# Optimization experiments

Measured on AMD Instinct MI355X. Metric: run time of the kernel, lower is better.

The kernel has to match this reference:

```python
import jax, jax.numpy as jnp
import numpy as np

N_NODES = 50000
N_EDGES = 400000
D_IN = 512
D_OUT = 512


def setup_inputs() -> dict:
    key = jax.random.key(0)
    k1, k2, k3, k4, k5 = jax.random.split(key, 5)
    x = jax.random.normal(k1, (N_NODES, D_IN), dtype=jnp.float32)
    adj_rows = jax.random.randint(k2, (N_EDGES,), 0, N_NODES, dtype=jnp.int32)
    adj_cols = jax.random.randint(k3, (N_EDGES,), 0, N_NODES, dtype=jnp.int32)
    adj_vals = jax.random.uniform(k4, (N_EDGES,), dtype=jnp.float32)
    # Xavier uniform init for weight, zeros for bias (as in reset_parameters)
    limit = float(np.sqrt(6.0 / (D_IN + D_OUT)))
    weight = jax.random.uniform(k5, (D_IN, D_OUT), minval=-limit, maxval=limit, dtype=jnp.float32)
    bias = jnp.zeros((D_OUT,), dtype=jnp.float32)
    return {"x": x, "adj_rows": adj_rows, "adj_cols": adj_cols,
            "adj_vals": adj_vals, "weight": weight, "bias": bias}


def reference(x, adj_rows, adj_cols, adj_vals, weight, bias):
    # support = x @ W  : dense GEMM [N, D_in] x [D_in, D_out]
    support = jnp.matmul(x, weight)
    # output = spmm(adj, support): COO sparse-dense matmul via gather + segment_sum
    messages = adj_vals[:, None] * support[adj_cols]  # [E, D_out]
    output = jax.ops.segment_sum(messages, adj_rows, num_segments=N_NODES)
    return output + bias
```

## Files before the change

### kernel.cpp

```cpp
#include <hip/hip_runtime.h>

#define N_NODES 50000
#define N_EDGES 400000
#define DIM 512
#define NPAD 50048
#define MTILES 391
#define NTILES 4
#define LDP 40

typedef short  short8  __attribute__((ext_vector_type(8)));
typedef unsigned short ushort8 __attribute__((ext_vector_type(8)));
typedef float  f32x4   __attribute__((ext_vector_type(4)));

__device__ __forceinline__ unsigned short f2bf(float f) {
    unsigned int u = __float_as_uint(f);
    u += 0x7fffu + ((u >> 16) & 1u);
    return (unsigned short)(u >> 16);
}
__device__ __forceinline__ float bf2f(unsigned short h) {
    return __uint_as_float(((unsigned int)h) << 16);
}

__global__ __launch_bounds__(256) void cast_x_kernel(const float* __restrict__ x,
                                                     unsigned short* __restrict__ xb) {
    size_t t = (size_t)blockIdx.x * 256 + threadIdx.x;
    size_t base = t * 8;
    int row = (int)(base >> 9);
    ushort8 o;
    if (row < N_NODES) {
        f32x4 a = *(const f32x4*)(x + base);
        f32x4 b = *(const f32x4*)(x + base + 4);
        o[0] = f2bf(a[0]); o[1] = f2bf(a[1]); o[2] = f2bf(a[2]); o[3] = f2bf(a[3]);
        o[4] = f2bf(b[0]); o[5] = f2bf(b[1]); o[6] = f2bf(b[2]); o[7] = f2bf(b[3]);
    } else {
        #pragma unroll
        for (int q = 0; q < 8; ++q) o[q] = 0;
    }
    *(ushort8*)(xb + base) = o;
}

__global__ __launch_bounds__(256) void cast_wt_kernel(const float* __restrict__ w,
                                                      unsigned short* __restrict__ wt) {
    int t = blockIdx.x * 256 + threadIdx.x;
    int n = t >> 9, k = t & 511;
    wt[t] = f2bf(w[k * 512 + n]);
}

__global__ __launch_bounds__(256) void hist_kernel(const int* __restrict__ rows,
                                                   int* __restrict__ counts) {
    int e = blockIdx.x * 256 + threadIdx.x;
    if (e < N_EDGES) atomicAdd(&counts[rows[e]], 1);
}

__global__ __launch_bounds__(512) void scan_blocks_kernel(const int* __restrict__ counts,
                                                          int* __restrict__ tmp,
                                                          int* __restrict__ partials) {
    __shared__ int sm[512];
    int i = blockIdx.x * 512 + threadIdx.x;
    int v = (i < N_NODES) ? counts[i] : 0;
    sm[threadIdx.x] = v;
    __syncthreads();
    #pragma unroll
    for (int off = 1; off < 512; off <<= 1) {
        int val = 0;
        if ((int)threadIdx.x >= off) val = sm[threadIdx.x - off];
        __syncthreads();
        if ((int)threadIdx.x >= off) sm[threadIdx.x] += val;
        __syncthreads();
    }
    if (i < N_NODES) tmp[i] = sm[threadIdx.x] - v;
    if (threadIdx.x == 511) partials[blockIdx.x] = sm[511];
}

__global__ __launch_bounds__(128) void scan_partials_kernel(int* __restrict__ partials) {
    __shared__ int sm[128];
    const int nb = 98;
    int v = ((int)threadIdx.x < nb) ? partials[threadIdx.x] : 0;
    sm[threadIdx.x] = v;
    __syncthreads();
    #pragma unroll
    for (int off = 1; off < 128; off <<= 1) {
        int val = 0;
        if ((int)threadIdx.x >= off) val = sm[threadIdx.x - off];
        __syncthreads();
        if ((int)threadIdx.x >= off) sm[threadIdx.x] += val;
        __syncthreads();
    }
    if ((int)threadIdx.x < nb) partials[threadIdx.x] = sm[threadIdx.x] - v;
}

__global__ __launch_bounds__(256) void add_offsets_kernel(const int* __restrict__ tmp,
                                                          const int* __restrict__ partials,
                                                          int* __restrict__ row_start,
                                                          int* __restrict__ cursor) {
    int i = blockIdx.x * 256 + threadIdx.x;
    if (i < N_NODES) {
        int rs = tmp[i] + partials[i >> 9];
        row_start[i] = rs;
        cursor[i] = rs;
    }
}

__global__ __launch_bounds__(256) void scatter_kernel(const int* __restrict__ rows,
                                                      const int* __restrict__ cols,
                                                      const float* __restrict__ vals,
                                                      int* __restrict__ cursor,
                                                      int* __restrict__ csr_col,
                                                      float* __restrict__ csr_val) {
    int e = blockIdx.x * 256 + threadIdx.x;
    if (e < N_EDGES) {
        int r = rows[e];
        int p = atomicAdd(&cursor[r], 1);
        csr_col[p] = cols[e];
        csr_val[p] = vals[e];
    }
}

__global__ __launch_bounds__(256) void gemm_kernel(const unsigned short* __restrict__ Xb,
                                                   const unsigned short* __restrict__ Wt,
                                                   unsigned short* __restrict__ S) {
    __shared__ __align__(16) unsigned short As[128 * LDP];
    __shared__ __align__(16) unsigned short Bs[128 * LDP];
    const int m0 = blockIdx.y * 128;
    const int n0 = blockIdx.x * 128;
    const int t = threadIdx.x;
    const int lane = t & 63;
    const int w = t >> 6;
    const int wr = w >> 1, wc = w & 1;
    const int fr = lane & 15;
    const int kg = lane >> 4;

    f32x4 acc[4][4];
    #pragma unroll
    for (int i = 0; i < 4; ++i)
        #pragma unroll
        for (int j = 0; j < 4; ++j)
            #pragma unroll
            for (int q = 0; q < 4; ++q) acc[i][j][q] = 0.0f;

    const int c0 = t, c1 = t + 256;
    const int ar0 = c0 >> 2, ak0 = c0 & 3;
    const int ar1 = c1 >> 2, ak1 = c1 & 3;

    for (int kk = 0; kk < DIM; kk += 32) {
        __syncthreads();
        *(f32x4*)&As[ar0 * LDP + ak0 * 8] = *(const f32x4*)&Xb[(size_t)(m0 + ar0) * DIM + kk + ak0 * 8];
        *(f32x4*)&As[ar1 * LDP + ak1 * 8] = *(const f32x4*)&Xb[(size_t)(m0 + ar1) * DIM + kk + ak1 * 8];
        *(f32x4*)&Bs[ar0 * LDP + ak0 * 8] = *(const f32x4*)&Wt[(size_t)(n0 + ar0) * DIM + kk + ak0 * 8];
        *(f32x4*)&Bs[ar1 * LDP + ak1 * 8] = *(const f32x4*)&Wt[(size_t)(n0 + ar1) * DIM + kk + ak1 * 8];
        __syncthreads();

        short8 af[4], bf[4];
        #pragma unroll
        for (int mi = 0; mi < 4; ++mi)
            af[mi] = *(const short8*)&As[(wr * 64 + mi * 16 + fr) * LDP + kg * 8];
        #pragma unroll
        for (int ni = 0; ni < 4; ++ni)
            bf[ni] = *(const short8*)&Bs[(wc * 64 + ni * 16 + fr) * LDP + kg * 8];

        #pragma unroll
        for (int mi = 0; mi < 4; ++mi)
            #pragma unroll
            for (int ni = 0; ni < 4; ++ni)
                acc[mi][ni] = __builtin_amdgcn_mfma_f32_16x16x32_bf16(af[mi], bf[ni], acc[mi][ni], 0, 0, 0);
    }

    #pragma unroll
    for (int mi = 0; mi < 4; ++mi) {
        #pragma unroll
        for (int ni = 0; ni < 4; ++ni) {
            int gr = m0 + wr * 64 + mi * 16 + kg * 4;
            int gc = n0 + wc * 64 + ni * 16 + fr;
            #pragma unroll
            for (int j = 0; j < 4; ++j)
                S[(size_t)(gr + j) * DIM + gc] = f2bf(acc[mi][ni][j]);
        }
    }
}

__global__ __launch_bounds__(64) void spmm_kernel(const unsigned short* __restrict__ S,
                                                  const int* __restrict__ row_start,
                                                  const int* __restrict__ counts,
                                                  const int* __restrict__ csr_col,
                                                  const float* __restrict__ csr_val,
                                                  const float* __restrict__ bias,
                                                  float* __restrict__ out) {
    const int r = blockIdx.x;
    const int lane = threadIdx.x;
    const int s = row_start[r];
    const int n = counts[r];
    float acc[8];
    #pragma unroll
    for (int q = 0; q < 8; ++q) acc[q] = 0.0f;

    for (int j = 0; j < n; ++j) {
        int c = csr_col[s + j];
        float v = csr_val[s + j];
        ushort8 sv = *(const ushort8*)&S[(size_t)c * DIM + lane * 8];
        #pragma unroll
        for (int q = 0; q < 8; ++q) acc[q] += v * bf2f(sv[q]);
    }
    #pragma unroll
    for (int q = 0; q < 8; ++q) acc[q] += bias[lane * 8 + q];

    f32x4 o0, o1;
    #pragma unroll
    for (int q = 0; q < 4; ++q) { o0[q] = acc[q]; o1[q] = acc[4 + q]; }
    *(f32x4*)&out[(size_t)r * DIM + lane * 8] = o0;
    *(f32x4*)&out[(size_t)r * DIM + lane * 8 + 4] = o1;
}

extern "C" void kernel_launch(void* const* d_in, const int* in_sizes, int n_in,
                              void* d_out, int out_size, void* d_ws, size_t ws_size,
                              hipStream_t stream) {
    const float* x    = (const float*)d_in[0];
    const int*   rows = (const int*)d_in[1];
    const int*   cols = (const int*)d_in[2];
    const float* vals = (const float*)d_in[3];
    const float* w    = (const float*)d_in[4];
    const float* bias = (const float*)d_in[5];
    float* out = (float*)d_out;

    char* ws = (char*)d_ws;
    size_t off = 0;
    auto alloc = [&](size_t bytes) -> char* {
        char* p = ws + off;
        off = (off + bytes + 255) & ~(size_t)255;
        return p;
    };
    unsigned short* Xb      = (unsigned short*)alloc((size_t)NPAD * DIM * 2);
    unsigned short* Wt      = (unsigned short*)alloc((size_t)DIM * DIM * 2);
    unsigned short* S       = (unsigned short*)alloc((size_t)NPAD * DIM * 2);
    int*            counts  = (int*)alloc((size_t)N_NODES * 4);
    int*            tmp     = (int*)alloc((size_t)N_NODES * 4);
    int*            rstart  = (int*)alloc((size_t)N_NODES * 4);
    int*            cursor  = (int*)alloc((size_t)N_NODES * 4);
    int*            partials= (int*)alloc(512);
    int*            csr_col = (int*)alloc((size_t)N_EDGES * 4);
    float*          csr_val = (float*)alloc((size_t)N_EDGES * 4);

    hipMemsetAsync(counts, 0, (size_t)N_NODES * 4, stream);

    cast_x_kernel<<<(NPAD * DIM / 8) / 256, 256, 0, stream>>>(x, Xb);
    cast_wt_kernel<<<(DIM * DIM) / 256, 256, 0, stream>>>(w, Wt);

    hist_kernel<<<(N_EDGES + 255) / 256, 256, 0, stream>>>(rows, counts);
    scan_blocks_kernel<<<98, 512, 0, stream>>>(counts, tmp, partials);
    scan_partials_kernel<<<1, 128, 0, stream>>>(partials);
    add_offsets_kernel<<<(N_NODES + 255) / 256, 256, 0, stream>>>(tmp, partials, rstart, cursor);
    scatter_kernel<<<(N_EDGES + 255) / 256, 256, 0, stream>>>(rows, cols, vals, cursor, csr_col, csr_val);

    gemm_kernel<<<dim3(NTILES, MTILES), 256, 0, stream>>>(Xb, Wt, S);
    spmm_kernel<<<N_NODES, 64, 0, stream>>>(S, rstart, counts, csr_col, csr_val, bias, out);
}
```

Baseline: 356.6 us.

## Use direct global-to-LDS loads in GEMM, pack CSR pairs, unroll SpMM gathers

The GEMM now stages tiles with global_load_lds straight into unpadded LDS instead of going through registers, and moves the barrier to the end of each k-step. The CSR column and value arrays are interleaved into one int2 array, and the SpMM loop is unrolled by four so four independent row gathers are in flight at once, with out-of-range slots masked to column 0 and value 0. Output stores become nontemporal. Without padding, LDS reads in the GEMM may hit bank conflicts, and the unrolled loop reads up to three entries past a row's end, which the extra allocation padding is meant to cover.

```diff
diff --git a/kernel.cpp b/kernel.cpp
--- a/kernel.cpp
+++ b/kernel.cpp
@@ -6,11 +6,14 @@
 #define NPAD 50048
 #define MTILES 391
 #define NTILES 4
-#define LDP 40
 
 typedef short  short8  __attribute__((ext_vector_type(8)));
 typedef unsigned short ushort8 __attribute__((ext_vector_type(8)));
 typedef float  f32x4   __attribute__((ext_vector_type(4)));
+typedef int    int2v   __attribute__((ext_vector_type(2)));
+
+typedef __attribute__((address_space(1))) const unsigned short gu16;
+typedef __attribute__((address_space(3))) unsigned short lu16;
 
 __device__ __forceinline__ unsigned short f2bf(float f) {
     unsigned int u = __float_as_uint(f);
@@ -105,22 +108,23 @@
                                                       const int* __restrict__ cols,
                                                       const float* __restrict__ vals,
                                                       int* __restrict__ cursor,
-                                                      int* __restrict__ csr_col,
-                                                      float* __restrict__ csr_val) {
+                                                      int2v* __restrict__ csr_cv) {
     int e = blockIdx.x * 256 + threadIdx.x;
     if (e < N_EDGES) {
         int r = rows[e];
         int p = atomicAdd(&cursor[r], 1);
-        csr_col[p] = cols[e];
-        csr_val[p] = vals[e];
+        int2v cv;
+        cv[0] = cols[e];
+        cv[1] = __float_as_int(vals[e]);
+        csr_cv[p] = cv;
     }
 }
 
 __global__ __launch_bounds__(256) void gemm_kernel(const unsigned short* __restrict__ Xb,
                                                    const unsigned short* __restrict__ Wt,
                                                    unsigned short* __restrict__ S) {
-    __shared__ __align__(16) unsigned short As[128 * LDP];
-    __shared__ __align__(16) unsigned short Bs[128 * LDP];
+    __shared__ __align__(16) unsigned short As[128 * 32];
+    __shared__ __align__(16) unsigned short Bs[128 * 32];
     const int m0 = blockIdx.y * 128;
     const int n0 = blockIdx.x * 128;
     const int t = threadIdx.x;
@@ -138,31 +142,39 @@
             #pragma unroll
             for (int q = 0; q < 4; ++q) acc[i][j][q] = 0.0f;
 
-    const int c0 = t, c1 = t + 256;
-    const int ar0 = c0 >> 2, ak0 = c0 & 3;
-    const int ar1 = c1 >> 2, ak1 = c1 & 3;
+    const int row0 = w * 16 + (lane >> 2);
+    const int row1 = row0 + 64;
+    const int col0 = (lane & 3) * 8;
+    lu16* AsW = (lu16*)(As + w * 512);
+    lu16* BsW = (lu16*)(Bs + w * 512);
+
+    const unsigned short* gA0 = Xb + (size_t)(m0 + row0) * DIM + col0;
+    const unsigned short* gA1 = Xb + (size_t)(m0 + row1) * DIM + col0;
+    const unsigned short* gB0 = Wt + (size_t)(n0 + row0) * DIM + col0;
+    const unsigned short* gB1 = Wt + (size_t)(n0 + row1) * DIM + col0;
 
     for (int kk = 0; kk < DIM; kk += 32) {
-        __syncthreads();
-        *(f32x4*)&As[ar0 * LDP + ak0 * 8] = *(const f32x4*)&Xb[(size_t)(m0 + ar0) * DIM + kk + ak0 * 8];
-        *(f32x4*)&As[ar1 * LDP + ak1 * 8] = *(const f32x4*)&Xb[(size_t)(m0 + ar1) * DIM + kk + ak1 * 8];
-        *(f32x4*)&Bs[ar0 * LDP + ak0 * 8] = *(const f32x4*)&Wt[(size_t)(n0 + ar0) * DIM + kk + ak0 * 8];
-        *(f32x4*)&Bs[ar1 * LDP + ak1 * 8] = *(const f32x4*)&Wt[(size_t)(n0 + ar1) * DIM + kk + ak1 * 8];
+        __builtin_amdgcn_global_load_lds((gu16*)(gA0 + kk), AsW,        16, 0, 0);
+        __builtin_amdgcn_global_load_lds((gu16*)(gA1 + kk), AsW + 2048, 16, 0, 0);
+        __builtin_amdgcn_global_load_lds((gu16*)(gB0 + kk), BsW,        16, 0, 0);
+        __builtin_amdgcn_global_load_lds((gu16*)(gB1 + kk), BsW + 2048, 16, 0, 0);
         __syncthreads();
 
         short8 af[4], bf[4];
         #pragma unroll
         for (int mi = 0; mi < 4; ++mi)
-            af[mi] = *(const short8*)&As[(wr * 64 + mi * 16 + fr) * LDP + kg * 8];
+            af[mi] = *(const short8*)&As[(wr * 64 + mi * 16 + fr) * 32 + kg * 8];
         #pragma unroll
         for (int ni = 0; ni < 4; ++ni)
-            bf[ni] = *(const short8*)&Bs[(wc * 64 + ni * 16 + fr) * LDP + kg * 8];
+            bf[ni] = *(const short8*)&Bs[(wc * 64 + ni * 16 + fr) * 32 + kg * 8];
 
         #pragma unroll
         for (int mi = 0; mi < 4; ++mi)
             #pragma unroll
             for (int ni = 0; ni < 4; ++ni)
                 acc[mi][ni] = __builtin_amdgcn_mfma_f32_16x16x32_bf16(af[mi], bf[ni], acc[mi][ni], 0, 0, 0);
+
+        __syncthreads();
     }
 
     #pragma unroll
@@ -181,33 +193,53 @@
 __global__ __launch_bounds__(64) void spmm_kernel(const unsigned short* __restrict__ S,
                                                   const int* __restrict__ row_start,
                                                   const int* __restrict__ counts,
-                                                  const int* __restrict__ csr_col,
-                                                  const float* __restrict__ csr_val,
+                                                  const int2v* __restrict__ cv,
                                                   const float* __restrict__ bias,
                                                   float* __restrict__ out) {
     const int r = blockIdx.x;
     const int lane = threadIdx.x;
     const int s = row_start[r];
     const int n = counts[r];
+    const size_t lo = (size_t)lane * 8;
+
     float acc[8];
     #pragma unroll
     for (int q = 0; q < 8; ++q) acc[q] = 0.0f;
 
-    for (int j = 0; j < n; ++j) {
-        int c = csr_col[s + j];
-        float v = csr_val[s + j];
-        ushort8 sv = *(const ushort8*)&S[(size_t)c * DIM + lane * 8];
-        #pragma unroll
-        for (int q = 0; q < 8; ++q) acc[q] += v * bf2f(sv[q]);
-    }
+    for (int j = 0; j < n; j += 4) {
+        int2v e0 = cv[s + j];
+        int2v e1 = cv[s + j + 1];
+        int2v e2 = cv[s + j + 2];
+        int2v e3 = cv[s + j + 3];
+        int c0 = e0[0];
+        int c1 = (j + 1 < n) ? e1[0] : 0;
+        int c2 = (j + 2 < n) ? e2[0] : 0;
+        int c3 = (j + 3 < n) ? e3[0] : 0;
+        float v0 = __int_as_float(e0[1]);
+        float v1 = (j + 1 < n) ? __int_as_float(e1[1]) : 0.0f;
+        float v2 = (j + 2 < n) ? __int_as_float(e2[1]) : 0.0f;
+        float v3 = (j + 3 < n) ? __int_as_float(e3[1]) : 0.0f;
+        ushort8 x0 = *(const ushort8*)&S[(size_t)c0 * DIM + lo];
+        ushort8 x1 = *(const ushort8*)&S[(size_t)c1 * DIM + lo];
+        ushort8 x2 = *(const ushort8*)&S[(size_t)c2 * DIM + lo];
+        ushort8 x3 = *(const ushort8*)&S[(size_t)c3 * DIM + lo];
+        #pragma unroll
+        for (int q = 0; q < 8; ++q) {
+            acc[q] += v0 * bf2f(x0[q]);
+            acc[q] += v1 * bf2f(x1[q]);
+            acc[q] += v2 * bf2f(x2[q]);
+            acc[q] += v3 * bf2f(x3[q]);
+        }
+    }
+
     #pragma unroll
     for (int q = 0; q < 8; ++q) acc[q] += bias[lane * 8 + q];
 
     f32x4 o0, o1;
     #pragma unroll
     for (int q = 0; q < 4; ++q) { o0[q] = acc[q]; o1[q] = acc[4 + q]; }
-    *(f32x4*)&out[(size_t)r * DIM + lane * 8] = o0;
-    *(f32x4*)&out[(size_t)r * DIM + lane * 8 + 4] = o1;
+    __builtin_nontemporal_store(o0, (f32x4*)&out[(size_t)r * DIM + lo]);
+    __builtin_nontemporal_store(o1, (f32x4*)&out[(size_t)r * DIM + lo + 4]);
 }
 
 extern "C" void kernel_launch(void* const* d_in, const int* in_sizes, int n_in,
@@ -236,8 +268,7 @@
     int*            rstart  = (int*)alloc((size_t)N_NODES * 4);
     int*            cursor  = (int*)alloc((size_t)N_NODES * 4);
     int*            partials= (int*)alloc(512);
-    int*            csr_col = (int*)alloc((size_t)N_EDGES * 4);
-    float*          csr_val = (float*)alloc((size_t)N_EDGES * 4);
+    int2v*          csr_cv  = (int2v*)alloc((size_t)(N_EDGES + 8) * 8);
 
     hipMemsetAsync(counts, 0, (size_t)N_NODES * 4, stream);
 
@@ -248,8 +279,8 @@
     scan_blocks_kernel<<<98, 512, 0, stream>>>(counts, tmp, partials);
     scan_partials_kernel<<<1, 128, 0, stream>>>(partials);
     add_offsets_kernel<<<(N_NODES + 255) / 256, 256, 0, stream>>>(tmp, partials, rstart, cursor);
-    scatter_kernel<<<(N_EDGES + 255) / 256, 256, 0, stream>>>(rows, cols, vals, cursor, csr_col, csr_val);
+    scatter_kernel<<<(N_EDGES + 255) / 256, 256, 0, stream>>>(rows, cols, vals, cursor, csr_cv);
 
     gemm_kernel<<<dim3(NTILES, MTILES), 256, 0, stream>>>(Xb, Wt, S);
-    spmm_kernel<<<N_NODES, 64, 0, stream>>>(S, rstart, counts, csr_col, csr_val, bias, out);
-}
+    spmm_kernel<<<N_NODES, 64, 0, stream>>>(S, rstart, counts, csr_cv, bias, out);
+}
```

Result: no change. 353.9 us (-0.8%).
